# Performance work log

Measured on AMD Instinct MI355X. Metric: run time of the kernel, lower is better.

## Reference

```python
import jax, jax.numpy as jnp
import numpy as np

H = 192      # hidden size
B = 8        # number of trees (perfect binary trees)
L = 32       # leaves per tree (must be power of 2)
VOC = 32000  # vocabulary size
OUT = 5      # output classes (SST-5)


def setup_inputs() -> dict:
    key = jax.random.key(0)
    ks = jax.random.split(key, 6)
    s = 1.0 / np.sqrt(2 * H)
    return {
        "embed": jax.random.normal(ks[0], (VOC, H), jnp.float32) * 0.02,
        "Vt": jax.random.normal(ks[1], (H, 2 * H, 2 * H), jnp.float32) * s,  # stacked V list
        "W": jax.random.normal(ks[2], (2 * H, H), jnp.float32) * s,
        "b": jnp.zeros((1, H), jnp.float32),
        "Wout_w": jax.random.normal(ks[3], (OUT, H), jnp.float32) * 0.05,
        "Wout_b": jnp.zeros((OUT,), jnp.float32),
        "leaf_ids": jax.random.randint(ks[4], (B, L), 0, VOC),
    }


def reference(embed, Vt, W, b, Wout_w, Wout_b, leaf_ids):
    # Leaves: embedding lookup. [B, L, H]
    cur = embed[leaf_ids]
    nodes = [cur.reshape(-1, H)]
    # Process tree levels bottom-up; adjacent pairs are (left, right) siblings.
    while cur.shape[1] > 1:
        n = cur.shape[1]
        # concat([left, right], feature dim): [B, n//2, 2H]
        c = cur.reshape(cur.shape[0], n // 2, 2 * H)
        # bilinear slice products: x^T V_h x for each h -> [B, n//2, H]
        xVx = jnp.einsum('bnx,hxy,bny->bnh', c, Vt, c)
        Wx = jnp.einsum('bnx,xh->bnh', c, W)
        cur = jnp.tanh(xVx + Wx + b)  # b broadcasts [1, H]
        nodes.append(cur.reshape(-1, H))
    allv = jnp.concatenate(nodes, axis=0)  # [B*(2L-1), H]
    logits = allv @ Wout_w.T + Wout_b
    return jax.nn.log_softmax(logits, axis=-1)
```

## Files before the change

kernel.cpp:

```cpp
#include <hip/hip_runtime.h>
#include <hip/hip_bf16.h>

#define HD 192
#define H2 384
#define NOUT 5

typedef __attribute__((ext_vector_type(4))) float f32x4;
typedef __attribute__((ext_vector_type(8))) short bf16x8;
typedef long long ll;

__device__ __forceinline__ ushort f2bf(float f) {
    union { float f; unsigned u; } v; v.f = f;
    unsigned r = v.u + 0x7FFF + ((v.u >> 16) & 1);
    return (ushort)(r >> 16);
}
__device__ __forceinline__ float bf2f(ushort s) {
    union { unsigned u; float f; } v; v.u = ((unsigned)s) << 16;
    return v.f;
}

__global__ void leaf_kernel(const float* __restrict__ embed, const int* __restrict__ leaf_ids,
                            float* __restrict__ nodes, ushort* __restrict__ C1,
                            ushort* __restrict__ C5, float* __restrict__ xA) {
    int r = blockIdx.x;
    int t = threadIdx.x;
    int id = leaf_ids[r];
    float v = embed[(ll)id * HD + t];
    nodes[r * HD + t] = v;
    C1[r * HD + t] = f2bf(v);
    int idx = r * HD + t;
    if (idx < HD * 128) xA[idx] = 0.f;
    if (r == 0) {
        for (int i = t; i < 8 * H2; i += HD) C5[8 * H2 + i] = 0;
    }
}

template<int NT, bool CVT>
__global__ __launch_bounds__(256) void gemm_kernel(const void* __restrict__ Av,
        const ushort* __restrict__ C, float* __restrict__ xVx, ushort* __restrict__ VtbOut) {
    constexpr int NP = NT * 16;
    __shared__ ushort Clds[NP * 200];
    __shared__ float red[4][NP];
    const int tid = threadIdx.x, lane = tid & 63, wave = tid >> 6;
    const int blk = blockIdx.x;
    const int m0 = blk * 128 + wave * 32;
    const int h  = blk / 3;
    const int x0 = (blk % 3) * 128;
    const int lr = lane & 15, dr = (lane >> 4) * 4, lk = (lane >> 4) * 8;

    f32x4 acc[2][NT];
#pragma unroll
    for (int mi = 0; mi < 2; mi++)
#pragma unroll
        for (int ni = 0; ni < NT; ni++) acc[mi][ni] = (f32x4){0.f, 0.f, 0.f, 0.f};

#pragma unroll
    for (int kh = 0; kh < 2; kh++) {
        __syncthreads();
        for (int i = tid; i < NP * 24; i += 256) {
            int row = i / 24, c8 = (i % 24) * 8;
            *(uint4*)&Clds[row * 200 + c8] = *(const uint4*)&C[row * H2 + kh * 192 + c8];
        }
        __syncthreads();
#pragma unroll
        for (int kk = 0; kk < 6; kk++) {
            const int k0 = kk * 32, kg = kh * 192 + k0;
            bf16x8 a[2], b[NT];
#pragma unroll
            for (int mi = 0; mi < 2; mi++) {
                const ll rowoff = (ll)(m0 + mi * 16 + lr) * H2 + kg + lk;
                if constexpr (CVT) {
                    const float* ap = (const float*)Av + rowoff;
                    float4 u0 = *(const float4*)ap;
                    float4 u1 = *(const float4*)(ap + 4);
                    bf16x8 f;
                    f[0] = (short)f2bf(u0.x); f[1] = (short)f2bf(u0.y);
                    f[2] = (short)f2bf(u0.z); f[3] = (short)f2bf(u0.w);
                    f[4] = (short)f2bf(u1.x); f[5] = (short)f2bf(u1.y);
                    f[6] = (short)f2bf(u1.z); f[7] = (short)f2bf(u1.w);
                    a[mi] = f;
                    *(bf16x8*)&VtbOut[rowoff] = f;
                } else {
                    a[mi] = *(const bf16x8*)&((const ushort*)Av)[rowoff];
                }
            }
#pragma unroll
            for (int ni = 0; ni < NT; ni++)
                b[ni] = *(const bf16x8*)&Clds[(ni * 16 + lr) * 200 + k0 + lk];
#pragma unroll
            for (int mi = 0; mi < 2; mi++)
#pragma unroll
                for (int ni = 0; ni < NT; ni++)
                    acc[mi][ni] = __builtin_amdgcn_mfma_f32_16x16x32_bf16(a[mi], b[ni], acc[mi][ni], 0, 0, 0);
        }
    }
    float part[NT];
#pragma unroll
    for (int ni = 0; ni < NT; ni++) {
        float p = 0.f;
#pragma unroll
        for (int mi = 0; mi < 2; mi++) {
            int xb = x0 + wave * 32 + mi * 16 + dr;
            ushort4 cv = *(const ushort4*)&C[(ni * 16 + lr) * H2 + xb];
            p += acc[mi][ni][0] * bf2f(cv.x) + acc[mi][ni][1] * bf2f(cv.y)
               + acc[mi][ni][2] * bf2f(cv.z) + acc[mi][ni][3] * bf2f(cv.w);
        }
        p += __shfl_xor(p, 16);
        p += __shfl_xor(p, 32);
        part[ni] = p;
    }
    if (lane < 16) {
#pragma unroll
        for (int ni = 0; ni < NT; ni++) red[wave][ni * 16 + lane] = part[ni];
    }
    __syncthreads();
    if (tid < NP) {
        float s = red[0][tid] + red[1][tid] + red[2][tid] + red[3][tid];
        atomicAdd(&xVx[h * NP + tid], s);
    }
}

__global__ __launch_bounds__(256) void epilogue_kernel(const float* __restrict__ xVx,
        const ushort* __restrict__ C, const float* __restrict__ W, const float* __restrict__ bb,
        float* __restrict__ outn, ushort* __restrict__ Cnext,
        float* __restrict__ zbuf, int zcount, int N, int log2N, int NP) {
    const int h = blockIdx.x, tid = threadIdx.x;
    __shared__ float wl[H2];
    __shared__ float red[256];
    for (int x = tid; x < H2; x += 256) wl[x] = W[x * HD + h];
    __syncthreads();
    const int n = tid & (N - 1), xs = tid >> log2N, XS = 256 >> log2N;
    float a = 0.f;
    for (int x = xs; x < H2; x += XS) a += bf2f(C[n * H2 + x]) * wl[x];
    red[tid] = a;
    __syncthreads();
    for (int s = 128; s >= N; s >>= 1) {
        if (tid < s) red[tid] += red[tid + s];
        __syncthreads();
    }
    if (tid < N) {
        float pre = xVx[h * NP + tid] + red[tid] + bb[h];
        float t = tanhf(pre);
        outn[tid * HD + h] = t;
        if (Cnext) Cnext[tid * HD + h] = f2bf(t);
    }
    if (zbuf) {
        int idx = h * 256 + tid;
        if (idx < zcount) zbuf[idx] = 0.f;
    }
}

__global__ void logits_kernel(const float* __restrict__ nodes, const float* __restrict__ Ww,
                              const float* __restrict__ Wb, float* __restrict__ out) {
    int r = blockIdx.x, t = threadIdx.x;
    __shared__ float lg[NOUT];
    if (t < NOUT) {
        float s = Wb[t];
        const float* a = nodes + r * HD;
        const float* w = Ww + t * HD;
#pragma unroll 8
        for (int k = 0; k < HD; k++) s += a[k] * w[k];
        lg[t] = s;
    }
    __syncthreads();
    if (t < NOUT) {
        float m = lg[0];
        for (int i = 1; i < NOUT; i++) m = fmaxf(m, lg[i]);
        float sum = 0.f;
        for (int i = 0; i < NOUT; i++) sum += expf(lg[i] - m);
        out[r * NOUT + t] = lg[t] - m - logf(sum);
    }
}

extern "C" void kernel_launch(void* const* d_in, const int* in_sizes, int n_in,
                              void* d_out, int out_size, void* d_ws, size_t ws_size,
                              hipStream_t stream) {
    const float* embed    = (const float*)d_in[0];
    const float* Vt       = (const float*)d_in[1];
    const float* W        = (const float*)d_in[2];
    const float* bb       = (const float*)d_in[3];
    const float* Ww       = (const float*)d_in[4];
    const float* Wb       = (const float*)d_in[5];
    const int*   leaf_ids = (const int*)d_in[6];
    float* out = (float*)d_out;

    char* ws = (char*)d_ws;
    size_t off = 0;
    ushort* Vtb  = (ushort*)(ws + off); off += (size_t)73728 * H2 * 2;
    float*  nodes= (float*) (ws + off); off += (size_t)504 * HD * 4;
    ushort* C1   = (ushort*)(ws + off); off += (size_t)128 * H2 * 2;
    ushort* C2   = (ushort*)(ws + off); off += (size_t)64  * H2 * 2;
    ushort* C3   = (ushort*)(ws + off); off += (size_t)32  * H2 * 2;
    ushort* C4   = (ushort*)(ws + off); off += (size_t)16  * H2 * 2;
    ushort* C5   = (ushort*)(ws + off); off += (size_t)16  * H2 * 2;
    float*  xA   = (float*) (ws + off); off += (size_t)HD * 128 * 4;
    float*  xB   = (float*) (ws + off); off += (size_t)HD * 128 * 4;

    leaf_kernel<<<256, HD, 0, stream>>>(embed, leaf_ids, nodes, C1, C5, xA);

    gemm_kernel<8, true ><<<576, 256, 0, stream>>>(Vt,  C1, xA, Vtb);
    epilogue_kernel<<<HD, 256, 0, stream>>>(xA, C1, W, bb, nodes + 256 * HD, C2, xB, HD * 64, 128, 7, 128);
    gemm_kernel<4, false><<<576, 256, 0, stream>>>(Vtb, C2, xB, nullptr);
    epilogue_kernel<<<HD, 256, 0, stream>>>(xB, C2, W, bb, nodes + 384 * HD, C3, xA, HD * 32, 64, 6, 64);
    gemm_kernel<2, false><<<576, 256, 0, stream>>>(Vtb, C3, xA, nullptr);
    epilogue_kernel<<<HD, 256, 0, stream>>>(xA, C3, W, bb, nodes + 448 * HD, C4, xB, HD * 16, 32, 5, 32);
    gemm_kernel<1, false><<<576, 256, 0, stream>>>(Vtb, C4, xB, nullptr);
    epilogue_kernel<<<HD, 256, 0, stream>>>(xB, C4, W, bb, nodes + 480 * HD, C5, xA, HD * 16, 16, 4, 16);
    gemm_kernel<1, false><<<576, 256, 0, stream>>>(Vtb, C5, xA, nullptr);
    epilogue_kernel<<<HD, 256, 0, stream>>>(xA, C5, W, bb, nodes + 496 * HD, (ushort*)nullptr,
                                            (float*)nullptr, 0, 8, 3, 16);

    logits_kernel<<<504, 64, 0, stream>>>(nodes, Ww, Wb, out);
}
```

Baseline: 343.2 us.

## Split Vt conversion out, fold W term into bilinear GEMM, slim epilogue to tanh

Moves the fp32-to-bf16 conversion of Vt into a standalone streaming kernel instead of fusing it into the first level's GEMM. The per-level GEMM now uses 64-row tiles held in registers across the full K and reads C directly from global memory rather than staging it in LDS. It also folds the W·x linear term into the bilinear reduction by adding W[x,h] to V·x before the dot with x. The separate reduction epilogue becomes a trivial tanh kernel that also re-zeroes the single accumulation buffer. This removes the per-level epilogue matvec and a second scratch buffer, at the cost of an extra kernel launch, extra passes over Vt, and more atomics from the larger grid.

```diff
diff --git a/kernel.cpp b/kernel.cpp
--- a/kernel.cpp
+++ b/kernel.cpp
@@ -19,9 +19,22 @@
     return v.f;
 }
 
+__global__ __launch_bounds__(256) void convert_kernel(const float* __restrict__ src,
+                                                      ushort* __restrict__ dst) {
+    const ll base = (ll)blockIdx.x * (64 * H2);
+    for (int i = threadIdx.x; i < 3072; i += 256) {
+        ll e = base + (ll)i * 8;
+        float4 a = *(const float4*)(src + e);
+        float4 b = *(const float4*)(src + e + 4);
+        ushort o[8] = { f2bf(a.x), f2bf(a.y), f2bf(a.z), f2bf(a.w),
+                        f2bf(b.x), f2bf(b.y), f2bf(b.z), f2bf(b.w) };
+        *(uint4*)(dst + e) = *(uint4*)o;
+    }
+}
+
 __global__ void leaf_kernel(const float* __restrict__ embed, const int* __restrict__ leaf_ids,
                             float* __restrict__ nodes, ushort* __restrict__ C1,
-                            ushort* __restrict__ C5, float* __restrict__ xA) {
+                            ushort* __restrict__ C5, float* __restrict__ xbuf) {
     int r = blockIdx.x;
     int t = threadIdx.x;
     int id = leaf_ids[r];
@@ -29,124 +42,79 @@
     nodes[r * HD + t] = v;
     C1[r * HD + t] = f2bf(v);
     int idx = r * HD + t;
-    if (idx < HD * 128) xA[idx] = 0.f;
+    if (idx < HD * 128) xbuf[idx] = 0.f;
     if (r == 0) {
         for (int i = t; i < 8 * H2; i += HD) C5[8 * H2 + i] = 0;
     }
 }
 
-template<int NT, bool CVT>
-__global__ __launch_bounds__(256) void gemm_kernel(const void* __restrict__ Av,
-        const ushort* __restrict__ C, float* __restrict__ xVx, ushort* __restrict__ VtbOut) {
-    constexpr int NP = NT * 16;
-    __shared__ ushort Clds[NP * 200];
-    __shared__ float red[4][NP];
+template<int NT>
+__global__ __launch_bounds__(256, 4) void gemm_level_kernel(const ushort* __restrict__ Vtb,
+        const ushort* __restrict__ Cl, const float* __restrict__ W, float* __restrict__ xbuf) {
+    __shared__ float wl[64];
+    __shared__ float red[128];
     const int tid = threadIdx.x, lane = tid & 63, wave = tid >> 6;
     const int blk = blockIdx.x;
-    const int m0 = blk * 128 + wave * 32;
-    const int h  = blk / 3;
-    const int x0 = (blk % 3) * 128;
-    const int lr = lane & 15, dr = (lane >> 4) * 4, lk = (lane >> 4) * 8;
+    const int h = blk / 6, xb0 = (blk % 6) * 64;
+    const int lr = lane & 15, hi = lane >> 4, lk = hi * 8, dr = hi * 4;
 
-    f32x4 acc[2][NT];
+    if (tid < 64) wl[tid] = W[(xb0 + tid) * HD + h];
+
+    bf16x8 areg[12];
+    const ushort* arow = Vtb + ((ll)blk * 64 + wave * 16 + lr) * H2;
 #pragma unroll
-    for (int mi = 0; mi < 2; mi++)
+    for (int kk = 0; kk < 12; kk++) areg[kk] = *(const bf16x8*)&arow[kk * 32 + lk];
+    __syncthreads();
+
+    constexpr int CHUNK = (NT >= 2) ? 2 : 1;
 #pragma unroll
-        for (int ni = 0; ni < NT; ni++) acc[mi][ni] = (f32x4){0.f, 0.f, 0.f, 0.f};
-
+    for (int nc = 0; nc < NT / CHUNK; nc++) {
+        f32x4 acc[CHUNK];
 #pragma unroll
-    for (int kh = 0; kh < 2; kh++) {
-        __syncthreads();
-        for (int i = tid; i < NP * 24; i += 256) {
-            int row = i / 24, c8 = (i % 24) * 8;
-            *(uint4*)&Clds[row * 200 + c8] = *(const uint4*)&C[row * H2 + kh * 192 + c8];
+        for (int ci = 0; ci < CHUNK; ci++) acc[ci] = (f32x4){0.f, 0.f, 0.f, 0.f};
+#pragma unroll
+        for (int kk = 0; kk < 12; kk++) {
+#pragma unroll
+            for (int ci = 0; ci < CHUNK; ci++) {
+                bf16x8 b = *(const bf16x8*)&Cl[((nc * CHUNK + ci) * 16 + lr) * H2 + kk * 32 + lk];
+                acc[ci] = __builtin_amdgcn_mfma_f32_16x16x32_bf16(areg[kk], b, acc[ci], 0, 0, 0);
+            }
+        }
+        float part[CHUNK];
+#pragma unroll
+        for (int ci = 0; ci < CHUNK; ci++) {
+            int n = (nc * CHUNK + ci) * 16 + lr;
+            int loc = wave * 16 + dr;
+            ushort4 cv = *(const ushort4*)&Cl[n * H2 + xb0 + loc];
+            float4  wv = *(const float4*)&wl[loc];
+            float p = (acc[ci][0] + wv.x) * bf2f(cv.x) + (acc[ci][1] + wv.y) * bf2f(cv.y)
+                    + (acc[ci][2] + wv.z) * bf2f(cv.z) + (acc[ci][3] + wv.w) * bf2f(cv.w);
+            p += __shfl_xor(p, 16);
+            p += __shfl_xor(p, 32);
+            part[ci] = p;
         }
         __syncthreads();
+        if (lane < 16) {
 #pragma unroll
-        for (int kk = 0; kk < 6; kk++) {
-            const int k0 = kk * 32, kg = kh * 192 + k0;
-            bf16x8 a[2], b[NT];
-#pragma unroll
-            for (int mi = 0; mi < 2; mi++) {
-                const ll rowoff = (ll)(m0 + mi * 16 + lr) * H2 + kg + lk;
-                if constexpr (CVT) {
-                    const float* ap = (const float*)Av + rowoff;
-                    float4 u0 = *(const float4*)ap;
-                    float4 u1 = *(const float4*)(ap + 4);
-                    bf16x8 f;
-                    f[0] = (short)f2bf(u0.x); f[1] = (short)f2bf(u0.y);
-                    f[2] = (short)f2bf(u0.z); f[3] = (short)f2bf(u0.w);
-                    f[4] = (short)f2bf(u1.x); f[5] = (short)f2bf(u1.y);
-                    f[6] = (short)f2bf(u1.z); f[7] = (short)f2bf(u1.w);
-                    a[mi] = f;
-                    *(bf16x8*)&VtbOut[rowoff] = f;
-                } else {
-                    a[mi] = *(const bf16x8*)&((const ushort*)Av)[rowoff];
-                }
-            }
-#pragma unroll
-            for (int ni = 0; ni < NT; ni++)
-                b[ni] = *(const bf16x8*)&Clds[(ni * 16 + lr) * 200 + k0 + lk];
-#pragma unroll
-            for (int mi = 0; mi < 2; mi++)
-#pragma unroll
-                for (int ni = 0; ni < NT; ni++)
-                    acc[mi][ni] = __builtin_amdgcn_mfma_f32_16x16x32_bf16(a[mi], b[ni], acc[mi][ni], 0, 0, 0);
+            for (int ci = 0; ci < CHUNK; ci++) red[wave * 32 + ci * 16 + lane] = part[ci];
         }
-    }
-    float part[NT];
-#pragma unroll
-    for (int ni = 0; ni < NT; ni++) {
-        float p = 0.f;
-#pragma unroll
-        for (int mi = 0; mi < 2; mi++) {
-            int xb = x0 + wave * 32 + mi * 16 + dr;
-            ushort4 cv = *(const ushort4*)&C[(ni * 16 + lr) * H2 + xb];
-            p += acc[mi][ni][0] * bf2f(cv.x) + acc[mi][ni][1] * bf2f(cv.y)
-               + acc[mi][ni][2] * bf2f(cv.z) + acc[mi][ni][3] * bf2f(cv.w);
+        __syncthreads();
+        if (tid < CHUNK * 16) {
+            float s = red[tid] + red[32 + tid] + red[64 + tid] + red[96 + tid];
+            atomicAdd(&xbuf[h * 128 + nc * CHUNK * 16 + tid], s);
         }
-        p += __shfl_xor(p, 16);
-        p += __shfl_xor(p, 32);
-        part[ni] = p;
-    }
-    if (lane < 16) {
-#pragma unroll
-        for (int ni = 0; ni < NT; ni++) red[wave][ni * 16 + lane] = part[ni];
-    }
-    __syncthreads();
-    if (tid < NP) {
-        float s = red[0][tid] + red[1][tid] + red[2][tid] + red[3][tid];
-        atomicAdd(&xVx[h * NP + tid], s);
     }
 }
 
-__global__ __launch_bounds__(256) void epilogue_kernel(const float* __restrict__ xVx,
-        const ushort* __restrict__ C, const float* __restrict__ W, const float* __restrict__ bb,
-        float* __restrict__ outn, ushort* __restrict__ Cnext,
-        float* __restrict__ zbuf, int zcount, int N, int log2N, int NP) {
-    const int h = blockIdx.x, tid = threadIdx.x;
-    __shared__ float wl[H2];
-    __shared__ float red[256];
-    for (int x = tid; x < H2; x += 256) wl[x] = W[x * HD + h];
-    __syncthreads();
-    const int n = tid & (N - 1), xs = tid >> log2N, XS = 256 >> log2N;
-    float a = 0.f;
-    for (int x = xs; x < H2; x += XS) a += bf2f(C[n * H2 + x]) * wl[x];
-    red[tid] = a;
-    __syncthreads();
-    for (int s = 128; s >= N; s >>= 1) {
-        if (tid < s) red[tid] += red[tid + s];
-        __syncthreads();
-    }
-    if (tid < N) {
-        float pre = xVx[h * NP + tid] + red[tid] + bb[h];
-        float t = tanhf(pre);
-        outn[tid * HD + h] = t;
-        if (Cnext) Cnext[tid * HD + h] = f2bf(t);
-    }
-    if (zbuf) {
-        int idx = h * 256 + tid;
-        if (idx < zcount) zbuf[idx] = 0.f;
+__global__ void tanh_kernel(float* __restrict__ xbuf, const float* __restrict__ bvec,
+                            float* __restrict__ nodes_base, ushort* __restrict__ Cnext, int Nl) {
+    int hh = blockIdx.x, tid = threadIdx.x;
+    float v = xbuf[hh * 128 + tid];
+    xbuf[hh * 128 + tid] = 0.f;
+    if (tid < Nl) {
+        float t = tanhf(v + bvec[hh]);
+        nodes_base[tid * HD + hh] = t;
+        if (Cnext) Cnext[(tid >> 1) * H2 + (tid & 1) * HD + hh] = f2bf(t);
     }
 }
 
@@ -178,7 +146,7 @@
     const float* embed    = (const float*)d_in[0];
     const float* Vt       = (const float*)d_in[1];
     const float* W        = (const float*)d_in[2];
-    const float* bb       = (const float*)d_in[3];
+    const float* bvec     = (const float*)d_in[3];
     const float* Ww       = (const float*)d_in[4];
     const float* Wb       = (const float*)d_in[5];
     const int*   leaf_ids = (const int*)d_in[6];
@@ -193,22 +161,21 @@
     ushort* C3   = (ushort*)(ws + off); off += (size_t)32  * H2 * 2;
     ushort* C4   = (ushort*)(ws + off); off += (size_t)16  * H2 * 2;
     ushort* C5   = (ushort*)(ws + off); off += (size_t)16  * H2 * 2;
-    float*  xA   = (float*) (ws + off); off += (size_t)HD * 128 * 4;
-    float*  xB   = (float*) (ws + off); off += (size_t)HD * 128 * 4;
+    float*  X    = (float*) (ws + off); off += (size_t)HD * 128 * 4;
 
-    leaf_kernel<<<256, HD, 0, stream>>>(embed, leaf_ids, nodes, C1, C5, xA);
+    convert_kernel<<<1152, 256, 0, stream>>>(Vt, Vtb);
+    leaf_kernel<<<256, HD, 0, stream>>>(embed, leaf_ids, nodes, C1, C5, X);
 
-    gemm_kernel<8, true ><<<576, 256, 0, stream>>>(Vt,  C1, xA, Vtb);
-    epilogue_kernel<<<HD, 256, 0, stream>>>(xA, C1, W, bb, nodes + 256 * HD, C2, xB, HD * 64, 128, 7, 128);
-    gemm_kernel<4, false><<<576, 256, 0, stream>>>(Vtb, C2, xB, nullptr);
-    epilogue_kernel<<<HD, 256, 0, stream>>>(xB, C2, W, bb, nodes + 384 * HD, C3, xA, HD * 32, 64, 6, 64);
-    gemm_kernel<2, false><<<576, 256, 0, stream>>>(Vtb, C3, xA, nullptr);
-    epilogue_kernel<<<HD, 256, 0, stream>>>(xA, C3, W, bb, nodes + 448 * HD, C4, xB, HD * 16, 32, 5, 32);
-    gemm_kernel<1, false><<<576, 256, 0, stream>>>(Vtb, C4, xB, nullptr);
-    epilogue_kernel<<<HD, 256, 0, stream>>>(xB, C4, W, bb, nodes + 480 * HD, C5, xA, HD * 16, 16, 4, 16);
-    gemm_kernel<1, false><<<576, 256, 0, stream>>>(Vtb, C5, xA, nullptr);
-    epilogue_kernel<<<HD, 256, 0, stream>>>(xA, C5, W, bb, nodes + 496 * HD, (ushort*)nullptr,
-                                            (float*)nullptr, 0, 8, 3, 16);
+    gemm_level_kernel<8><<<1152, 256, 0, stream>>>(Vtb, C1, W, X);
+    tanh_kernel<<<HD, 128, 0, stream>>>(X, bvec, nodes + 256 * HD, C2, 128);
+    gemm_level_kernel<4><<<1152, 256, 0, stream>>>(Vtb, C2, W, X);
+    tanh_kernel<<<HD, 128, 0, stream>>>(X, bvec, nodes + 384 * HD, C3, 64);
+    gemm_level_kernel<2><<<1152, 256, 0, stream>>>(Vtb, C3, W, X);
+    tanh_kernel<<<HD, 128, 0, stream>>>(X, bvec, nodes + 448 * HD, C4, 32);
+    gemm_level_kernel<1><<<1152, 256, 0, stream>>>(Vtb, C4, W, X);
+    tanh_kernel<<<HD, 128, 0, stream>>>(X, bvec, nodes + 480 * HD, C5, 16);
+    gemm_level_kernel<1><<<1152, 256, 0, stream>>>(Vtb, C5, W, X);
+    tanh_kernel<<<HD, 128, 0, stream>>>(X, bvec, nodes + 496 * HD, (ushort*)nullptr, 8);
 
     logits_kernel<<<504, 64, 0, stream>>>(nodes, Ww, Wb, out);
 }
```

Measured after the change: 378.6 us. 10.3% more time.
